# Performance work log

Measured on AMD Instinct MI355X. Metric: run time of the kernel, lower is better.

## Reference

```python
import jax, jax.numpy as jnp
import numpy as np

H = 8          # heads
D = 512        # d_model
DK = D // H    # per-head dim
FF = 2048      # feed-forward size
STACKS = 3
VOCAB = 5000
PAD = 0
LN_EPS = 1e-6


def _layer_norm(x, g, b):
    mu = jnp.mean(x, axis=-1, keepdims=True)
    var = jnp.mean(jnp.square(x - mu), axis=-1, keepdims=True)
    return (x - mu) * jax.lax.rsqrt(var + LN_EPS) * g + b


def _positional_encoding(T, d):
    pos = jnp.arange(T, dtype=jnp.float32)[:, None]                      # (T,1)
    div = jnp.exp(jnp.arange(0, d, 2, dtype=jnp.float32) * (-np.log(10000.0) / d))
    pe = jnp.zeros((T, d), dtype=jnp.float32)
    pe = pe.at[:, 0::2].set(jnp.sin(pos * div))
    pe = pe.at[:, 1::2].set(jnp.cos(pos * div))
    return pe  # (T, D)


def _mha(q_in, kv, wq, bq, wk, bk, wv, bv, wo, bo, mask):
    B, Tq, _ = q_in.shape
    Tk = kv.shape[1]
    q = (q_in @ wq + bq).reshape(B, Tq, H, DK).transpose(0, 2, 1, 3)   # (B,H,Tq,DK)
    k = (kv @ wk + bk).reshape(B, Tk, H, DK).transpose(0, 2, 1, 3)
    v = (kv @ wv + bv).reshape(B, Tk, H, DK).transpose(0, 2, 1, 3)
    score = jnp.einsum('bhqd,bhkd->bhqk', q, k) / jnp.sqrt(jnp.float32(DK))
    if mask is not None:
        score = jnp.where(mask, score, jnp.float32(-1e9))
    p = jax.nn.softmax(score, axis=-1)
    out = jnp.einsum('bhqk,bhkd->bhqd', p, v)
    out = out.transpose(0, 2, 1, 3).reshape(B, Tq, D)
    return out @ wo + bo


def setup_inputs() -> dict:
    key = jax.random.key(0)
    ks = jax.random.split(key, 24)
    s = 0.02
    inp = {
        'target': jax.random.randint(ks[0], (32, 256), 0, VOCAB),
        'memory': jax.random.normal(ks[1], (32, 1024, D), dtype=jnp.float32),
        'emb': jax.random.normal(ks[2], (VOCAB, D), dtype=jnp.float32) * s,
        'ln_g': jnp.ones((D,), jnp.float32),
        'ln_b': jnp.zeros((D,), jnp.float32),
        'ff_w1': jax.random.normal(ks[3], (D, FF), jnp.float32) * s,
        'ff_b1': jnp.zeros((FF,), jnp.float32),
        'ff_w2': jax.random.normal(ks[4], (FF, D), jnp.float32) * s,
        'ff_b2': jnp.zeros((D,), jnp.float32),
    }
    names = ['wq', 'wk', 'wv', 'wo']
    for i, n in enumerate(names):
        inp['sa_' + n] = jax.random.normal(ks[5 + i], (D, D), jnp.float32) * s
        inp['sa_b' + n[1]] = jnp.zeros((D,), jnp.float32)
        inp['ca_' + n] = jax.random.normal(ks[9 + i], (D, D), jnp.float32) * s
        inp['ca_b' + n[1]] = jnp.zeros((D,), jnp.float32)
    return inp


def reference(target, memory, emb, ln_g, ln_b, ff_w1, ff_b1, ff_w2, ff_b2,
              sa_wq, sa_bq, sa_wk, sa_bk, sa_wv, sa_bv, sa_wo, sa_bo,
              ca_wq, ca_bq, ca_wk, ca_bk, ca_wv, ca_bv, ca_wo, ca_bo):
    B, T = target.shape
    x = emb[target] * jnp.sqrt(jnp.float32(D))              # (B,T,D)
    x = x + _positional_encoding(T, D)                       # dropout = identity (eval)
    # masks: causal & pad for self-attn; cross-attn mask is all-ones -> skip
    pad = (target != PAD)[:, None, :, None]                  # (B,1,T,1)
    causal = jnp.tril(jnp.ones((T, T), dtype=bool))          # (T,T)
    tgt_mask = pad & causal                                  # (B,1,T,T)
    out = x
    for _ in range(STACKS):  # shared parameters
        n = _layer_norm(out, ln_g, ln_b)
        out = out + _mha(n, n, sa_wq, sa_bq, sa_wk, sa_bk, sa_wv, sa_bv, sa_wo, sa_bo, tgt_mask)
        n = _layer_norm(out, ln_g, ln_b)
        out = out + _mha(n, memory, ca_wq, ca_bq, ca_wk, ca_bk, ca_wv, ca_bv, ca_wo, ca_bo, None)
        n = _layer_norm(out, ln_g, ln_b)
        out = out + (jax.nn.relu(n @ ff_w1 + ff_b1) @ ff_w2 + ff_b2)
    return _layer_norm(out, ln_g, ln_b)
```

## Files before the change

### kernel.cpp

```cpp
#include <hip/hip_runtime.h>
#include <cstdint>
#include <cstddef>

typedef unsigned short u16;
typedef __bf16 bf16x8 __attribute__((ext_vector_type(8)));
typedef float f32x4 __attribute__((ext_vector_type(4)));

#define DEV static __device__ __forceinline__

#define QSCALE 0.18033688011112042f

DEV u16 f2bf(float f) { unsigned v; __builtin_memcpy(&v, &f, 4); v += 0x7fffu + ((v >> 16) & 1u); return (u16)(v >> 16); }

DEV void gll16(const void* g, void* l) {
    __builtin_amdgcn_global_load_lds(
        (__attribute__((address_space(1))) void*)g,
        (__attribute__((address_space(3))) void*)l, 16, 0, 0);
}

__global__ void embed_pe(const int* __restrict__ tgt, const float* __restrict__ emb,
                         float* __restrict__ x)
{
    const int bt = blockIdx.x;
    const int t  = bt & 255;
    const int tok = tgt[bt];
    for (int d = threadIdx.x; d < 512; d += 256) {
        float e  = emb[(size_t)tok * 512 + d] * 22.62741699796952f;
        int   d0 = d & ~1;
        float ang = (float)t * expf((float)d0 * (-9.210340371976184f / 512.f));
        float pe  = (d & 1) ? cosf(ang) : sinf(ang);
        x[(size_t)bt * 512 + d] = e + pe;
    }
}

__global__ void transpose_k(const float* __restrict__ in, u16* __restrict__ out,
                            int K, int N)
{
    int id = blockIdx.x * 256 + threadIdx.x;
    int k = id / N, n = id % N;
    out[(size_t)n * K + k] = f2bf(in[id]);
}

__global__ void memcast(const float* __restrict__ in, u16* __restrict__ out)
{
    int i = (blockIdx.x * 256 + threadIdx.x) * 4;
    float4 v = *(const float4*)(in + i);
    uint2 w;
    w.x = (unsigned)f2bf(v.x) | ((unsigned)f2bf(v.y) << 16);
    w.y = (unsigned)f2bf(v.z) | ((unsigned)f2bf(v.w) << 16);
    *(uint2*)(out + i) = w;
}

__global__ void concat_bias(const float* __restrict__ a, const float* __restrict__ b,
                            float* __restrict__ out)
{
    int i = blockIdx.x * 256 + threadIdx.x;
    if (i < 512) { out[i] = a[i]; out[512 + i] = b[i]; }
}

template<bool OUTF32>
__global__ void layernorm_k(const float* __restrict__ x, const float* __restrict__ g,
                            const float* __restrict__ b, void* __restrict__ outv)
{
    const int row  = blockIdx.x * 4 + (threadIdx.x >> 6);
    const int lane = threadIdx.x & 63;
    const float* xr = x + (size_t)row * 512;
    float4 v0 = *(const float4*)(xr + lane * 4);
    float4 v1 = *(const float4*)(xr + 256 + lane * 4);
    float s = v0.x + v0.y + v0.z + v0.w + v1.x + v1.y + v1.z + v1.w;
    float q = v0.x*v0.x + v0.y*v0.y + v0.z*v0.z + v0.w*v0.w
            + v1.x*v1.x + v1.y*v1.y + v1.z*v1.z + v1.w*v1.w;
#pragma unroll
    for (int o = 1; o < 64; o <<= 1) { s += __shfl_xor(s, o, 64); q += __shfl_xor(q, o, 64); }
    float mu  = s * (1.f / 512.f);
    float var = q * (1.f / 512.f) - mu * mu;
    float rs  = rsqrtf(fmaxf(var, 0.f) + 1e-6f);

#pragma unroll
    for (int h = 0; h < 2; h++) {
        const int d0 = h * 256 + lane * 4;
        float4 v = h ? v1 : v0;
        float4 gg = *(const float4*)(g + d0);
        float4 bb = *(const float4*)(b + d0);
        float o0 = (v.x - mu) * rs * gg.x + bb.x;
        float o1 = (v.y - mu) * rs * gg.y + bb.y;
        float o2 = (v.z - mu) * rs * gg.z + bb.z;
        float o3 = (v.w - mu) * rs * gg.w + bb.w;
        if (OUTF32) {
            *(float4*)((float*)outv + (size_t)row * 512 + d0) = make_float4(o0, o1, o2, o3);
        } else {
            uint2 w;
            w.x = (unsigned)f2bf(o0) | ((unsigned)f2bf(o1) << 16);
            w.y = (unsigned)f2bf(o2) | ((unsigned)f2bf(o3) << 16);
            *(uint2*)((u16*)outv + (size_t)row * 512 + d0) = w;
        }
    }
}

template<bool OUTF32>
__global__ void ln_sum_k(const float* __restrict__ x, const float* __restrict__ p,
                         const float* __restrict__ g, const float* __restrict__ b,
                         float* __restrict__ xout, void* __restrict__ outv)
{
    const int row  = blockIdx.x * 4 + (threadIdx.x >> 6);
    const int lane = threadIdx.x & 63;
    const size_t base = (size_t)row * 512;
    const float* xr = x + base;
    const float* pa = p + base;
    const float* pb = p + 4194304 + base;
    float4 v0, v1;
    {
        float4 a = *(const float4*)(xr + lane * 4);
        float4 c = *(const float4*)(pa + lane * 4);
        float4 d = *(const float4*)(pb + lane * 4);
        v0 = make_float4(a.x + c.x + d.x, a.y + c.y + d.y, a.z + c.z + d.z, a.w + c.w + d.w);
        a = *(const float4*)(xr + 256 + lane * 4);
        c = *(const float4*)(pa + 256 + lane * 4);
        d = *(const float4*)(pb + 256 + lane * 4);
        v1 = make_float4(a.x + c.x + d.x, a.y + c.y + d.y, a.z + c.z + d.z, a.w + c.w + d.w);
    }
    float s = v0.x + v0.y + v0.z + v0.w + v1.x + v1.y + v1.z + v1.w;
    float q = v0.x*v0.x + v0.y*v0.y + v0.z*v0.z + v0.w*v0.w
            + v1.x*v1.x + v1.y*v1.y + v1.z*v1.z + v1.w*v1.w;
#pragma unroll
    for (int o = 1; o < 64; o <<= 1) { s += __shfl_xor(s, o, 64); q += __shfl_xor(q, o, 64); }
    float mu  = s * (1.f / 512.f);
    float var = q * (1.f / 512.f) - mu * mu;
    float rs  = rsqrtf(fmaxf(var, 0.f) + 1e-6f);

#pragma unroll
    for (int h = 0; h < 2; h++) {
        const int d0 = h * 256 + lane * 4;
        float4 v = h ? v1 : v0;
        if (!OUTF32) *(float4*)(xout + base + d0) = v;
        float4 gg = *(const float4*)(g + d0);
        float4 bb = *(const float4*)(b + d0);
        float o0 = (v.x - mu) * rs * gg.x + bb.x;
        float o1 = (v.y - mu) * rs * gg.y + bb.y;
        float o2 = (v.z - mu) * rs * gg.z + bb.z;
        float o3 = (v.w - mu) * rs * gg.w + bb.w;
        if (OUTF32) {
            *(float4*)((float*)outv + base + d0) = make_float4(o0, o1, o2, o3);
        } else {
            uint2 w;
            w.x = (unsigned)f2bf(o0) | ((unsigned)f2bf(o1) << 16);
            w.y = (unsigned)f2bf(o2) | ((unsigned)f2bf(o3) << 16);
            *(uint2*)((u16*)outv + base + d0) = w;
        }
    }
}

template<int EPI, bool BROW, int BN, int QS, int SPLIT>
__launch_bounds__(256, BN == 64 ? 4 : 2)
__global__ void gemm_bt(const u16* __restrict__ A, int lda,
                        const u16* __restrict__ Bt,
                        const float* __restrict__ bias,
                        void* __restrict__ outp, int ldo, int K)
{
    constexpr int NJ = BN / 32;
    __shared__ u16 As[128 * 32];
    __shared__ u16 Bs[BN * 32];

    const int gx = gridDim.x, gy = gridDim.y;
    const int nwg = gx * gy * gridDim.z;
    int lin = blockIdx.x + gx * (blockIdx.y + gy * blockIdx.z);
    lin = (lin & 7) * (nwg >> 3) + (lin >> 3);
    const int bx = lin % gx;
    const int rem = lin / gx;
    const int by = rem % gy;
    const int bz = rem / gy;

    const int tid  = threadIdx.x;
    const int lane = tid & 63;
    const int wave = tid >> 6;
    const int quad = lane >> 4, l16 = lane & 15;
    const int l4 = lane >> 2, c8 = (lane & 3) * 8;
    const int m0 = by * 128, n0 = bx * BN;
    const int wm = (wave >> 1) * 64, wn = (wave & 1) * (BN / 2);

    const int kc = K / SPLIT;
    const int kbeg = bz * kc;

    f32x4 acc[4][NJ];
#pragma unroll
    for (int i = 0; i < 4; i++)
#pragma unroll
        for (int j = 0; j < NJ; j++) acc[i][j] = f32x4{0.f, 0.f, 0.f, 0.f};

    for (int k0 = kbeg; k0 < kbeg + kc; k0 += 32) {
        __syncthreads();
        gll16(&A[(size_t)(m0 + wave * 32 + l4)      * lda + k0 + c8], &As[(wave * 32) * 32]);
        gll16(&A[(size_t)(m0 + wave * 32 + 16 + l4) * lda + k0 + c8], &As[(wave * 32 + 16) * 32]);
        if (BN == 128) {
            gll16(&Bt[(size_t)(n0 + wave * 32 + l4)      * K + k0 + c8], &Bs[(wave * 32) * 32]);
            gll16(&Bt[(size_t)(n0 + wave * 32 + 16 + l4) * K + k0 + c8], &Bs[(wave * 32 + 16) * 32]);
        } else {
            gll16(&Bt[(size_t)(n0 + wave * 16 + l4) * K + k0 + c8], &Bs[(wave * 16) * 32]);
        }
        __syncthreads();
        bf16x8 af[4], bfr[NJ];
#pragma unroll
        for (int i = 0; i < 4; i++) af[i]  = *(const bf16x8*)&As[(wm + i * 16 + l16) * 32 + quad * 8];
#pragma unroll
        for (int j = 0; j < NJ; j++) bfr[j] = *(const bf16x8*)&Bs[(wn + j * 16 + l16) * 32 + quad * 8];
#pragma unroll
        for (int i = 0; i < 4; i++)
#pragma unroll
            for (int j = 0; j < NJ; j++)
                acc[i][j] = __builtin_amdgcn_mfma_f32_16x16x32_bf16(af[i], bfr[j], acc[i][j], 0, 0, 0);
    }

    const bool dobias = (SPLIT == 1) || (bz == 0);
#pragma unroll
    for (int i = 0; i < 4; i++)
#pragma unroll
        for (int j = 0; j < NJ; j++) {
            const int col = n0 + wn + j * 16 + l16;
            const float bc = BROW ? 0.f : (dobias ? bias[col] : 0.f);
#pragma unroll
            for (int r = 0; r < 4; r++) {
                const int row = m0 + wm + i * 16 + quad * 4 + r;
                const float bv = BROW ? (dobias ? bias[row] : 0.f) : bc;
                float v = acc[i][j][r] + bv;
                if (QS == 1) v *= QSCALE;
                if (QS == 2 && col < 512) v *= QSCALE;
                if (EPI == 1) v = fmaxf(v, 0.f);
                if (EPI == 3) {
                    ((float*)outp)[(size_t)bz * 8192 * ldo + (size_t)row * ldo + col] = v;
                } else {
                    ((u16*)outp)[(size_t)row * ldo + col] = f2bf(v);
                }
            }
        }
}

template<bool SELF>
__launch_bounds__(512, 4)
__global__ void attn(const u16* __restrict__ Qb, int qs,
                     const u16* __restrict__ Kb, int ks, int koff,
                     const u16* __restrict__ Vt, int ldv,
                     const int* __restrict__ target,
                     u16* __restrict__ Ob, int Tk)
{
    __shared__ u16 KV[2][4][64 * 32];
    __shared__ __align__(16) __bf16 P16[8][16 * 72];
    __shared__ int needtail;
    const int tid  = threadIdx.x;
    const int lane = tid & 63;
    const int wave = tid >> 6;
    const int quad = lane >> 4, l16 = lane & 15;
    const int b = blockIdx.x, h = blockIdx.y, qz = blockIdx.z;
    const int qbase = qz * 128 + wave * 16;
    const int hq = h * 64;
    const int kcol = ((quad ^ ((l16 >> 1) & 3)) * 8);

    if (tid == 0) needtail = 0;

    const u16* qr = Qb + (size_t)(b * 256 + qbase + l16) * qs + hq;
    bf16x8 qf0 = *(const bf16x8*)(qr + quad * 8);
    bf16x8 qf1 = *(const bf16x8*)(qr + 32 + quad * 8);

    f32x4 o[4];
#pragma unroll
    for (int t = 0; t < 4; t++) o[t] = f32x4{0.f, 0.f, 0.f, 0.f};
    float pr[4] = {0.f, 0.f, 0.f, 0.f};

    bool rv[4];
    bool tpad = false;
    if (SELF) {
        bool inv = false;
#pragma unroll
        for (int r = 0; r < 4; r++) {
            rv[r] = (target[b * 256 + qbase + quad * 4 + r] != 0);
            inv |= !rv[r];
        }
        tpad = __any(inv);
    }

    const u16* kbase = Kb + (size_t)b * Tk * ks + koff + hq;
    const u16* vbase = Vt + (size_t)hq * ldv + (size_t)b * Tk;
    __bf16* pw = P16[wave];

    const int srow0 = ((wave * 2) & 3) * 16 + (lane >> 2);
    const int srow1 = ((wave * 2 + 1) & 3) * 16 + (lane >> 2);
    const int sc0 = (((lane & 3) ^ ((srow0 >> 1) & 3)) * 8);
    const int sc1 = (((lane & 3) ^ ((srow1 >> 1) & 3)) * 8);
    const int arr0 = (wave * 2) >> 2, arr1 = (wave * 2 + 1) >> 2;
    u16* ldst0;  u16* ldst1;

#define STAGE_KV(buf, k0)                                                        \
    {                                                                            \
        const u16* src0; const u16* src1;                                        \
        if (arr0 == 0)      src0 = kbase + (size_t)((k0) + srow0) * ks + sc0;    \
        else if (arr0 == 1) src0 = kbase + (size_t)((k0) + srow0) * ks + 32 + sc0;\
        else if (arr0 == 2) src0 = vbase + (size_t)srow0 * ldv + (k0) + sc0;     \
        else                src0 = vbase + (size_t)srow0 * ldv + (k0) + 32 + sc0;\
        if (arr1 == 0)      src1 = kbase + (size_t)((k0) + srow1) * ks + sc1;    \
        else if (arr1 == 1) src1 = kbase + (size_t)((k0) + srow1) * ks + 32 + sc1;\
        else if (arr1 == 2) src1 = vbase + (size_t)srow1 * ldv + (k0) + sc1;     \
        else                src1 = vbase + (size_t)srow1 * ldv + (k0) + 32 + sc1;\
        ldst0 = &KV[buf][arr0][(((wave * 2) & 3) * 16) * 32];                    \
        ldst1 = &KV[buf][arr1][(((wave * 2 + 1) & 3) * 16) * 32];                \
        gll16(src0, ldst0);                                                      \
        gll16(src1, ldst1);                                                      \
    }

    STAGE_KV(0, 0)
    __syncthreads();
    if (SELF && tpad && lane == 0) needtail = 1;
    __syncthreads();
    const int nch = SELF ? (needtail ? (Tk >> 6) : 2 * (qz + 1)) : (Tk >> 6);

    for (int c = 0; c < nch; c++) {
        const int cur = c & 1;
        const int k0 = c * 64;
        if (c + 1 < nch) STAGE_KV(cur ^ 1, (c + 1) * 64)

        const u16* KsLc = KV[cur][0];
        const u16* KsHc = KV[cur][1];
        const u16* VsLc = KV[cur][2];
        const u16* VsHc = KV[cur][3];

        const bool active = !SELF || (qbase + 16 > k0) || tpad;
        if (active) {
#pragma unroll
            for (int g = 0; g < 4; g++) {
                bf16x8 kf0 = *(const bf16x8*)&KsLc[(g * 16 + l16) * 32 + kcol];
                bf16x8 kf1 = *(const bf16x8*)&KsHc[(g * 16 + l16) * 32 + kcol];
                f32x4 sv = f32x4{0.f, 0.f, 0.f, 0.f};
                sv = __builtin_amdgcn_mfma_f32_16x16x32_bf16(qf0, kf0, sv, 0, 0, 0);
                sv = __builtin_amdgcn_mfma_f32_16x16x32_bf16(qf1, kf1, sv, 0, 0, 0);
                if (SELF) {
                    if (k0 + 64 > qbase) {
#pragma unroll
                        for (int r = 0; r < 4; r++)
                            if (k0 + g * 16 + l16 > qbase + quad * 4 + r) sv[r] = -1e9f;
                    }
                    if (tpad) {
#pragma unroll
                        for (int r = 0; r < 4; r++)
                            if (!rv[r]) sv[r] = 0.f;
                    }
                }
#pragma unroll
                for (int r = 0; r < 4; r++) {
                    float p = exp2f(sv[r]);
                    pr[r] += p;
                    pw[(quad * 4 + r) * 72 + g * 16 + l16] = (__bf16)p;
                }
            }
            bf16x8 pa0 = *(const bf16x8*)&pw[l16 * 72 + quad * 8];
            bf16x8 pa1 = *(const bf16x8*)&pw[l16 * 72 + 32 + quad * 8];
#pragma unroll
            for (int t = 0; t < 4; t++) {
                bf16x8 vf0 = *(const bf16x8*)&VsLc[(t * 16 + l16) * 32 + kcol];
                bf16x8 vf1 = *(const bf16x8*)&VsHc[(t * 16 + l16) * 32 + kcol];
                o[t] = __builtin_amdgcn_mfma_f32_16x16x32_bf16(pa0, vf0, o[t], 0, 0, 0);
                o[t] = __builtin_amdgcn_mfma_f32_16x16x32_bf16(pa1, vf1, o[t], 0, 0, 0);
            }
        }
        __syncthreads();
    }
#undef STAGE_KV

#pragma unroll
    for (int r = 0; r < 4; r++) {
#pragma unroll
        for (int off = 1; off < 16; off <<= 1) pr[r] += __shfl_xor(pr[r], off, 64);
    }
#pragma unroll
    for (int r = 0; r < 4; r++) {
        const float inv_l = 1.f / pr[r];
        const int tq = qbase + quad * 4 + r;
        u16* orow = Ob + (size_t)(b * 256 + tq) * 512 + hq;
#pragma unroll
        for (int t = 0; t < 4; t++) orow[t * 16 + l16] = f2bf(o[t][r] * inv_l);
    }
}

#define O_X      ((size_t)0)
#define O_N      ((size_t)16777216)
#define O_QK     ((size_t)25165824)
#define O_VTS    ((size_t)41943040)
#define O_ATT    ((size_t)50331648)
#define O_FFN    ((size_t)58720256)
#define O_KVC    ((size_t)92274688)
#define O_VTC    ((size_t)125829120)
#define O_WQKT   ((size_t)159383552)
#define O_SAVT   ((size_t)160432128)
#define O_WOT    ((size_t)160956416)
#define O_CAQT   ((size_t)161480704)
#define O_CAKT   ((size_t)162004992)
#define O_CAVT   ((size_t)162529280)
#define O_CAWOT  ((size_t)163053568)
#define O_FF1T   ((size_t)163577856)
#define O_FF2T   ((size_t)165675008)
#define O_BQK    ((size_t)167772160)

extern "C" void kernel_launch(void* const* d_in, const int* in_sizes, int n_in,
                              void* d_out, int out_size, void* d_ws, size_t ws_size,
                              hipStream_t stream)
{
    const int*   target = (const int*)d_in[0];
    const float* memory = (const float*)d_in[1];
    const float* emb    = (const float*)d_in[2];
    const float* ln_g   = (const float*)d_in[3];
    const float* ln_b   = (const float*)d_in[4];
    const float* ff_w1  = (const float*)d_in[5];
    const float* ff_b1  = (const float*)d_in[6];
    const float* ff_w2  = (const float*)d_in[7];
    const float* ff_b2  = (const float*)d_in[8];
    const float* sa_wq  = (const float*)d_in[9];
    const float* sa_bq  = (const float*)d_in[10];
    const float* ca_wq  = (const float*)d_in[11];
    const float* ca_bq  = (const float*)d_in[12];
    const float* sa_wk  = (const float*)d_in[13];
    const float* sa_bk  = (const float*)d_in[14];
    const float* ca_wk  = (const float*)d_in[15];
    const float* ca_bk  = (const float*)d_in[16];
    const float* sa_wv  = (const float*)d_in[17];
    const float* sa_bv  = (const float*)d_in[18];
    const float* ca_wv  = (const float*)d_in[19];
    const float* ca_bv  = (const float*)d_in[20];
    const float* sa_wo  = (const float*)d_in[21];
    const float* sa_bo  = (const float*)d_in[22];
    const float* ca_wo  = (const float*)d_in[23];
    const float* ca_bo  = (const float*)d_in[24];

    char* ws = (char*)d_ws;
    float* xf   = (float*)(ws + O_X);
    u16* nbuf   = (u16*)(ws + O_N);
    u16* qk     = (u16*)(ws + O_QK);
    u16* qbuf   = (u16*)(ws + O_QK);
    float* ffp  = (float*)(ws + O_QK);
    u16* vts    = (u16*)(ws + O_VTS);
    u16* att    = (u16*)(ws + O_ATT);
    u16* ffn    = (u16*)(ws + O_FFN);
    u16* membf  = (u16*)(ws + O_FFN);
    float* wop  = (float*)(ws + O_FFN);
    u16* kvc    = (u16*)(ws + O_KVC);
    u16* vtc    = (u16*)(ws + O_VTC);
    u16* wqkt   = (u16*)(ws + O_WQKT);
    u16* savt   = (u16*)(ws + O_SAVT);
    u16* wot    = (u16*)(ws + O_WOT);
    u16* caqt   = (u16*)(ws + O_CAQT);
    u16* cakt   = (u16*)(ws + O_CAKT);
    u16* cavt   = (u16*)(ws + O_CAVT);
    u16* cawot  = (u16*)(ws + O_CAWOT);
    u16* ff1t   = (u16*)(ws + O_FF1T);
    u16* ff2t   = (u16*)(ws + O_FF2T);
    float* bqk  = (float*)(ws + O_BQK);

    transpose_k<<<1024, 256, 0, stream>>>(sa_wq, wqkt,             512, 512);
    transpose_k<<<1024, 256, 0, stream>>>(sa_wk, wqkt + 512 * 512, 512, 512);
    transpose_k<<<1024, 256, 0, stream>>>(sa_wv, savt,  512, 512);
    transpose_k<<<1024, 256, 0, stream>>>(sa_wo, wot,   512, 512);
    transpose_k<<<1024, 256, 0, stream>>>(ca_wq, caqt,  512, 512);
    transpose_k<<<1024, 256, 0, stream>>>(ca_wk, cakt,  512, 512);
    transpose_k<<<1024, 256, 0, stream>>>(ca_wv, cavt,  512, 512);
    transpose_k<<<1024, 256, 0, stream>>>(ca_wo, cawot, 512, 512);
    transpose_k<<<4096, 256, 0, stream>>>(ff_w1, ff1t,  512, 2048);
    transpose_k<<<4096, 256, 0, stream>>>(ff_w2, ff2t, 2048, 512);
    concat_bias<<<2, 256, 0, stream>>>(sa_bq, sa_bk, bqk);

    embed_pe<<<8192, 256, 0, stream>>>(target, emb, xf);

    memcast<<<16384, 256, 0, stream>>>(memory, membf);
    gemm_bt<0, false, 64, 0, 1><<<dim3(8, 256), 256, 0, stream>>>(membf, 512, cakt, ca_bk, kvc, 512, 512);
    gemm_bt<0, true,  64, 0, 1><<<dim3(512, 4), 256, 0, stream>>>(cavt, 512, membf, ca_bv, vtc, 32768, 512);

    for (int s = 0; s < 3; s++) {
        if (s == 0)
            layernorm_k<false><<<2048, 256, 0, stream>>>(xf, ln_g, ln_b, nbuf);
        else
            ln_sum_k<false><<<2048, 256, 0, stream>>>(xf, ffp, ln_g, ln_b, xf, nbuf);
        gemm_bt<0, false, 64, 2, 1><<<dim3(16, 64), 256, 0, stream>>>(nbuf, 512, wqkt, bqk, qk, 1024, 512);
        gemm_bt<0, true,  64, 0, 1><<<dim3(128, 4), 256, 0, stream>>>(savt, 512, nbuf, sa_bv, vts, 8192, 512);
        attn<true><<<dim3(32, 8, 2), 512, 0, stream>>>(qk, 1024, qk, 1024, 512, vts, 8192, target, att, 256);
        gemm_bt<3, false, 64, 0, 2><<<dim3(8, 64, 2), 256, 0, stream>>>(att, 512, wot, sa_bo, wop, 512, 512);
        ln_sum_k<false><<<2048, 256, 0, stream>>>(xf, wop, ln_g, ln_b, xf, nbuf);
        gemm_bt<0, false, 64, 1, 1><<<dim3(8, 64), 256, 0, stream>>>(nbuf, 512, caqt, ca_bq, qbuf, 512, 512);
        attn<false><<<dim3(32, 8, 2), 512, 0, stream>>>(qbuf, 512, kvc, 512, 0, vtc, 32768, nullptr, att, 1024);
        gemm_bt<3, false, 64, 0, 2><<<dim3(8, 64, 2), 256, 0, stream>>>(att, 512, cawot, ca_bo, wop, 512, 512);
        ln_sum_k<false><<<2048, 256, 0, stream>>>(xf, wop, ln_g, ln_b, xf, nbuf);
        gemm_bt<1, false, 64, 0, 1><<<dim3(32, 64), 256, 0, stream>>>(nbuf, 512, ff1t, ff_b1, ffn, 2048, 512);
        gemm_bt<3, false, 64, 0, 2><<<dim3(8, 64, 2), 256, 0, stream>>>(ffn, 2048, ff2t, ff_b2, ffp, 512, 2048);
    }

    ln_sum_k<true><<<2048, 256, 0, stream>>>(xf, ffp, ln_g, ln_b, xf, d_out);
}
```

Before: 918.7 us.

## Keep attention probabilities in registers via transposed QK MFMA; shrink blocks to four waves

The attention kernel now computes S^T by swapping the MFMA operands and permutes the K rows it loads, so each lane's output probabilities already sit in the A-operand layout for the PV MFMA. This removes the per-wave LDS scratch buffer for P, along with its write/read round trip and intra-chunk dependency. Blocks drop from 8 to 4 waves (64 queries each) with twice as many blocks in z. Each wave now stages four K/V rows of the double buffer, and the row-sum reduction is simplified to two cross-quad shuffles. The trade-off is more blocks re-loading the same K/V tiles and a new swizzle whose correctness depends on the row permutation matching the MFMA layout.

```diff
diff --git a/kernel.cpp b/kernel.cpp
--- a/kernel.cpp
+++ b/kernel.cpp
@@ -235,7 +235,7 @@
 }
 
 template<bool SELF>
-__launch_bounds__(512, 4)
+__launch_bounds__(256, 4)
 __global__ void attn(const u16* __restrict__ Qb, int qs,
                      const u16* __restrict__ Kb, int ks, int koff,
                      const u16* __restrict__ Vt, int ldv,
@@ -243,16 +243,14 @@
                      u16* __restrict__ Ob, int Tk)
 {
     __shared__ u16 KV[2][4][64 * 32];
-    __shared__ __align__(16) __bf16 P16[8][16 * 72];
     __shared__ int needtail;
     const int tid  = threadIdx.x;
     const int lane = tid & 63;
     const int wave = tid >> 6;
     const int quad = lane >> 4, l16 = lane & 15;
     const int b = blockIdx.x, h = blockIdx.y, qz = blockIdx.z;
-    const int qbase = qz * 128 + wave * 16;
+    const int qbase = qz * 64 + wave * 16;
     const int hq = h * 64;
-    const int kcol = ((quad ^ ((l16 >> 1) & 3)) * 8);
 
     if (tid == 0) needtail = 0;
 
@@ -260,56 +258,65 @@
     bf16x8 qf0 = *(const bf16x8*)(qr + quad * 8);
     bf16x8 qf1 = *(const bf16x8*)(qr + 32 + quad * 8);
 
+    int koffs[4];
+    int okey[4];
+    {
+        const int p0 = 8 * (l16 >> 2) + (l16 & 3);
+        const int padd[4] = {0, 4, 32, 36};
+#pragma unroll
+        for (int g = 0; g < 4; g++) {
+            const int prow = p0 + padd[g];
+            const int sig = ((prow >> 1) ^ (prow >> 3)) & 3;
+            koffs[g] = prow * 32 + (quad ^ sig) * 8;
+            okey[g] = padd[g] + 8 * quad;
+        }
+    }
+    int voffs[4];
+#pragma unroll
+    for (int t = 0; t < 4; t++) {
+        const int row = t * 16 + l16;
+        const int sig = ((row >> 1) ^ (row >> 3)) & 3;
+        voffs[t] = row * 32 + (quad ^ sig) * 8;
+    }
+
     f32x4 o[4];
 #pragma unroll
     for (int t = 0; t < 4; t++) o[t] = f32x4{0.f, 0.f, 0.f, 0.f};
-    float pr[4] = {0.f, 0.f, 0.f, 0.f};
-
-    bool rv[4];
+    float ps = 0.f;
+
+    bool rvq = true;
     bool tpad = false;
     if (SELF) {
-        bool inv = false;
-#pragma unroll
-        for (int r = 0; r < 4; r++) {
-            rv[r] = (target[b * 256 + qbase + quad * 4 + r] != 0);
-            inv |= !rv[r];
-        }
-        tpad = __any(inv);
+        rvq = (target[b * 256 + qbase + l16] != 0);
+        tpad = __any(!rvq);
     }
 
     const u16* kbase = Kb + (size_t)b * Tk * ks + koff + hq;
     const u16* vbase = Vt + (size_t)hq * ldv + (size_t)b * Tk;
-    __bf16* pw = P16[wave];
-
-    const int srow0 = ((wave * 2) & 3) * 16 + (lane >> 2);
-    const int srow1 = ((wave * 2 + 1) & 3) * 16 + (lane >> 2);
-    const int sc0 = (((lane & 3) ^ ((srow0 >> 1) & 3)) * 8);
-    const int sc1 = (((lane & 3) ^ ((srow1 >> 1) & 3)) * 8);
-    const int arr0 = (wave * 2) >> 2, arr1 = (wave * 2 + 1) >> 2;
-    u16* ldst0;  u16* ldst1;
-
-#define STAGE_KV(buf, k0)                                                        \
-    {                                                                            \
-        const u16* src0; const u16* src1;                                        \
-        if (arr0 == 0)      src0 = kbase + (size_t)((k0) + srow0) * ks + sc0;    \
-        else if (arr0 == 1) src0 = kbase + (size_t)((k0) + srow0) * ks + 32 + sc0;\
-        else if (arr0 == 2) src0 = vbase + (size_t)srow0 * ldv + (k0) + sc0;     \
-        else                src0 = vbase + (size_t)srow0 * ldv + (k0) + 32 + sc0;\
-        if (arr1 == 0)      src1 = kbase + (size_t)((k0) + srow1) * ks + sc1;    \
-        else if (arr1 == 1) src1 = kbase + (size_t)((k0) + srow1) * ks + 32 + sc1;\
-        else if (arr1 == 2) src1 = vbase + (size_t)srow1 * ldv + (k0) + sc1;     \
-        else                src1 = vbase + (size_t)srow1 * ldv + (k0) + 32 + sc1;\
-        ldst0 = &KV[buf][arr0][(((wave * 2) & 3) * 16) * 32];                    \
-        ldst1 = &KV[buf][arr1][(((wave * 2 + 1) & 3) * 16) * 32];                \
-        gll16(src0, ldst0);                                                      \
-        gll16(src1, ldst1);                                                      \
+
+    const int sr = lane >> 2;
+    const int scb = (lane & 3) ^ ((sr >> 1) & 3);
+
+#define STAGE_KV(buf, k0)                                                     \
+    {                                                                         \
+        _Pragma("unroll")                                                     \
+        for (int j = 0; j < 4; j++) {                                         \
+            const int srow = j * 16 + sr;                                     \
+            const int sc = (scb ^ ((2 * j + (sr >> 3)) & 3)) * 8;             \
+            const u16* src;                                                   \
+            if (wave == 0)      src = kbase + (size_t)((k0) + srow) * ks + sc;     \
+            else if (wave == 1) src = kbase + (size_t)((k0) + srow) * ks + 32 + sc;\
+            else if (wave == 2) src = vbase + (size_t)srow * ldv + (k0) + sc;      \
+            else                src = vbase + (size_t)srow * ldv + (k0) + 32 + sc; \
+            gll16(src, &KV[buf][wave][(j * 16) * 32]);                        \
+        }                                                                     \
     }
 
     STAGE_KV(0, 0)
     __syncthreads();
     if (SELF && tpad && lane == 0) needtail = 1;
     __syncthreads();
-    const int nch = SELF ? (needtail ? (Tk >> 6) : 2 * (qz + 1)) : (Tk >> 6);
+    const int nch = SELF ? (needtail ? (Tk >> 6) : (qz + 1)) : (Tk >> 6);
 
     for (int c = 0; c < nch; c++) {
         const int cur = c & 1;
@@ -323,38 +330,35 @@
 
         const bool active = !SELF || (qbase + 16 > k0) || tpad;
         if (active) {
+            bf16x8 pa0, pa1;
 #pragma unroll
             for (int g = 0; g < 4; g++) {
-                bf16x8 kf0 = *(const bf16x8*)&KsLc[(g * 16 + l16) * 32 + kcol];
-                bf16x8 kf1 = *(const bf16x8*)&KsHc[(g * 16 + l16) * 32 + kcol];
+                bf16x8 kf0 = *(const bf16x8*)&KsLc[koffs[g]];
+                bf16x8 kf1 = *(const bf16x8*)&KsHc[koffs[g]];
                 f32x4 sv = f32x4{0.f, 0.f, 0.f, 0.f};
-                sv = __builtin_amdgcn_mfma_f32_16x16x32_bf16(qf0, kf0, sv, 0, 0, 0);
-                sv = __builtin_amdgcn_mfma_f32_16x16x32_bf16(qf1, kf1, sv, 0, 0, 0);
+                sv = __builtin_amdgcn_mfma_f32_16x16x32_bf16(kf0, qf0, sv, 0, 0, 0);
+                sv = __builtin_amdgcn_mfma_f32_16x16x32_bf16(kf1, qf1, sv, 0, 0, 0);
                 if (SELF) {
-                    if (k0 + 64 > qbase) {
-#pragma unroll
-                        for (int r = 0; r < 4; r++)
-                            if (k0 + g * 16 + l16 > qbase + quad * 4 + r) sv[r] = -1e9f;
-                    }
-                    if (tpad) {
-#pragma unroll
-                        for (int r = 0; r < 4; r++)
-                            if (!rv[r]) sv[r] = 0.f;
+#pragma unroll
+                    for (int r = 0; r < 4; r++) {
+                        if (k0 + okey[g] + r > qbase + l16) sv[r] = -1e9f;
+                        if (tpad && !rvq) sv[r] = 0.f;
                     }
                 }
 #pragma unroll
                 for (int r = 0; r < 4; r++) {
                     float p = exp2f(sv[r]);
-                    pr[r] += p;
-                    pw[(quad * 4 + r) * 72 + g * 16 + l16] = (__bf16)p;
+                    ps += p;
+                    if (g == 0)      pa0[r]     = (__bf16)p;
+                    else if (g == 1) pa0[4 + r] = (__bf16)p;
+                    else if (g == 2) pa1[r]     = (__bf16)p;
+                    else             pa1[4 + r] = (__bf16)p;
                 }
             }
-            bf16x8 pa0 = *(const bf16x8*)&pw[l16 * 72 + quad * 8];
-            bf16x8 pa1 = *(const bf16x8*)&pw[l16 * 72 + 32 + quad * 8];
 #pragma unroll
             for (int t = 0; t < 4; t++) {
-                bf16x8 vf0 = *(const bf16x8*)&VsLc[(t * 16 + l16) * 32 + kcol];
-                bf16x8 vf1 = *(const bf16x8*)&VsHc[(t * 16 + l16) * 32 + kcol];
+                bf16x8 vf0 = *(const bf16x8*)&VsLc[voffs[t]];
+                bf16x8 vf1 = *(const bf16x8*)&VsHc[voffs[t]];
                 o[t] = __builtin_amdgcn_mfma_f32_16x16x32_bf16(pa0, vf0, o[t], 0, 0, 0);
                 o[t] = __builtin_amdgcn_mfma_f32_16x16x32_bf16(pa1, vf1, o[t], 0, 0, 0);
             }
@@ -363,14 +367,11 @@
     }
 #undef STAGE_KV
 
+    ps += __shfl_xor(ps, 16, 64);
+    ps += __shfl_xor(ps, 32, 64);
 #pragma unroll
     for (int r = 0; r < 4; r++) {
-#pragma unroll
-        for (int off = 1; off < 16; off <<= 1) pr[r] += __shfl_xor(pr[r], off, 64);
-    }
-#pragma unroll
-    for (int r = 0; r < 4; r++) {
-        const float inv_l = 1.f / pr[r];
+        const float inv_l = 1.f / __shfl(ps, quad * 4 + r, 64);
         const int tq = qbase + quad * 4 + r;
         u16* orow = Ob + (size_t)(b * 256 + tq) * 512 + hq;
 #pragma unroll
@@ -476,11 +477,11 @@
             ln_sum_k<false><<<2048, 256, 0, stream>>>(xf, ffp, ln_g, ln_b, xf, nbuf);
         gemm_bt<0, false, 64, 2, 1><<<dim3(16, 64), 256, 0, stream>>>(nbuf, 512, wqkt, bqk, qk, 1024, 512);
         gemm_bt<0, true,  64, 0, 1><<<dim3(128, 4), 256, 0, stream>>>(savt, 512, nbuf, sa_bv, vts, 8192, 512);
-        attn<true><<<dim3(32, 8, 2), 512, 0, stream>>>(qk, 1024, qk, 1024, 512, vts, 8192, target, att, 256);
+        attn<true><<<dim3(32, 8, 4), 256, 0, stream>>>(qk, 1024, qk, 1024, 512, vts, 8192, target, att, 256);
         gemm_bt<3, false, 64, 0, 2><<<dim3(8, 64, 2), 256, 0, stream>>>(att, 512, wot, sa_bo, wop, 512, 512);
         ln_sum_k<false><<<2048, 256, 0, stream>>>(xf, wop, ln_g, ln_b, xf, nbuf);
         gemm_bt<0, false, 64, 1, 1><<<dim3(8, 64), 256, 0, stream>>>(nbuf, 512, caqt, ca_bq, qbuf, 512, 512);
-        attn<false><<<dim3(32, 8, 2), 512, 0, stream>>>(qbuf, 512, kvc, 512, 0, vtc, 32768, nullptr, att, 1024);
+        attn<false><<<dim3(32, 8, 4), 256, 0, stream>>>(qbuf, 512, kvc, 512, 0, vtc, 32768, nullptr, att, 1024);
         gemm_bt<3, false, 64, 0, 2><<<dim3(8, 64, 2), 256, 0, stream>>>(att, 512, cawot, ca_bo, wop, 512, 512);
         ln_sum_k<false><<<2048, 256, 0, stream>>>(xf, wop, ln_g, ln_b, xf, nbuf);
         gemm_bt<1, false, 64, 0, 1><<<dim3(32, 64), 256, 0, stream>>>(nbuf, 512, ff1t, ff_b1, ffn, 2048, 512);
```

Result: no change. 931.6 us (+1.4%).

## Double-buffer LDS tiles in bf16 GEMM to overlap global loads with MFMA

Applied to the files above, without the earlier changes.

The GEMM kernel now keeps two LDS buffers for the A and B tiles. It issues the asynchronous global-to-LDS loads for the next K step before running the MFMAs on the current buffer, with one barrier per iteration instead of two. The goal is to hide global memory latency behind compute and cut barrier overhead. In exchange, LDS use per workgroup doubles, which could limit occupancy, and the barrier must still drain the outstanding loads.

```diff
diff --git a/kernel.cpp b/kernel.cpp
--- a/kernel.cpp
+++ b/kernel.cpp
@@ -158,8 +158,8 @@
                         void* __restrict__ outp, int ldo, int K)
 {
     constexpr int NJ = BN / 32;
-    __shared__ u16 As[128 * 32];
-    __shared__ u16 Bs[BN * 32];
+    __shared__ u16 As[2][128 * 32];
+    __shared__ u16 Bs[2][BN * 32];
 
     const int gx = gridDim.x, gy = gridDim.y;
     const int nwg = gx * gy * gridDim.z;
@@ -180,6 +180,7 @@
 
     const int kc = K / SPLIT;
     const int kbeg = bz * kc;
+    const int nsteps = kc / 32;
 
     f32x4 acc[4][NJ];
 #pragma unroll
@@ -187,28 +188,39 @@
 #pragma unroll
         for (int j = 0; j < NJ; j++) acc[i][j] = f32x4{0.f, 0.f, 0.f, 0.f};
 
-    for (int k0 = kbeg; k0 < kbeg + kc; k0 += 32) {
-        __syncthreads();
-        gll16(&A[(size_t)(m0 + wave * 32 + l4)      * lda + k0 + c8], &As[(wave * 32) * 32]);
-        gll16(&A[(size_t)(m0 + wave * 32 + 16 + l4) * lda + k0 + c8], &As[(wave * 32 + 16) * 32]);
-        if (BN == 128) {
-            gll16(&Bt[(size_t)(n0 + wave * 32 + l4)      * K + k0 + c8], &Bs[(wave * 32) * 32]);
-            gll16(&Bt[(size_t)(n0 + wave * 32 + 16 + l4) * K + k0 + c8], &Bs[(wave * 32 + 16) * 32]);
-        } else {
-            gll16(&Bt[(size_t)(n0 + wave * 16 + l4) * K + k0 + c8], &Bs[(wave * 16) * 32]);
-        }
-        __syncthreads();
+#define GSTAGE(buf, kk)                                                                      \
+    {                                                                                        \
+        gll16(&A[(size_t)(m0 + wave * 32 + l4)      * lda + (kk) + c8], &As[buf][(wave * 32) * 32]);      \
+        gll16(&A[(size_t)(m0 + wave * 32 + 16 + l4) * lda + (kk) + c8], &As[buf][(wave * 32 + 16) * 32]); \
+        if (BN == 128) {                                                                     \
+            gll16(&Bt[(size_t)(n0 + wave * 32 + l4)      * K + (kk) + c8], &Bs[buf][(wave * 32) * 32]);      \
+            gll16(&Bt[(size_t)(n0 + wave * 32 + 16 + l4) * K + (kk) + c8], &Bs[buf][(wave * 32 + 16) * 32]); \
+        } else {                                                                             \
+            gll16(&Bt[(size_t)(n0 + wave * 16 + l4) * K + (kk) + c8], &Bs[buf][(wave * 16) * 32]);           \
+        }                                                                                    \
+    }
+
+    GSTAGE(0, kbeg)
+    __syncthreads();
+
+    for (int st = 0; st < nsteps; st++) {
+        const int cur = st & 1;
+        if (st + 1 < nsteps) GSTAGE(cur ^ 1, kbeg + (st + 1) * 32)
+
         bf16x8 af[4], bfr[NJ];
 #pragma unroll
-        for (int i = 0; i < 4; i++) af[i]  = *(const bf16x8*)&As[(wm + i * 16 + l16) * 32 + quad * 8];
-#pragma unroll
-        for (int j = 0; j < NJ; j++) bfr[j] = *(const bf16x8*)&Bs[(wn + j * 16 + l16) * 32 + quad * 8];
+        for (int i = 0; i < 4; i++) af[i]  = *(const bf16x8*)&As[cur][(wm + i * 16 + l16) * 32 + quad * 8];
+#pragma unroll
+        for (int j = 0; j < NJ; j++) bfr[j] = *(const bf16x8*)&Bs[cur][(wn + j * 16 + l16) * 32 + quad * 8];
 #pragma unroll
         for (int i = 0; i < 4; i++)
 #pragma unroll
             for (int j = 0; j < NJ; j++)
                 acc[i][j] = __builtin_amdgcn_mfma_f32_16x16x32_bf16(af[i], bfr[j], acc[i][j], 0, 0, 0);
-    }
+
+        __syncthreads();
+    }
+#undef GSTAGE
 
     const bool dobias = (SPLIT == 1) || (bz == 0);
 #pragma unroll
```

Result: no change. 916.9 us (-0.2%).
